# Kernel tuning notes

Hardware: AMD Instinct MI355X
Metric: run time of the kernel (lower is better)

Reference implementation:

```python
import jax, jax.numpy as jnp
import numpy as np
from jax import lax

WIN = 9          # window_size
EPS = 1e-08      # eps


def _box_filter(x):
    """Separable 3D box-mean filter (VALID), equivalent to conv3d with
    ones(WIN,WIN,WIN)/WIN**3. x: (B,1,D',H',W') padded volume."""
    for kshape in ((WIN, 1, 1), (1, WIN, 1), (1, 1, WIN)):
        k = jnp.ones((1, 1) + kshape, x.dtype) / WIN  # (O,I,kd,kh,kw)
        x = lax.conv_general_dilated(
            x, k, window_strides=(1, 1, 1), padding='VALID',
            dimension_numbers=('NCDHW', 'OIDHW', 'NCDHW'))
    return x


def setup_inputs() -> dict:
    key = jax.random.key(0)
    k1, k2 = jax.random.split(key)
    shape = (2, 1, 128, 128, 128)
    fixed = jax.random.uniform(k1, shape, dtype=jnp.float32)
    warped = jax.random.uniform(k2, shape, dtype=jnp.float32)
    return {"fixed": fixed, "warped": warped}


def reference(fixed, warped):
    pad = WIN // 2
    pw = [(0, 0), (0, 0), (pad, pad), (pad, pad), (pad, pad)]
    f = jnp.pad(fixed, pw, mode='reflect')
    w = jnp.pad(warped, pw, mode='reflect')

    mu_f = _box_filter(f)
    mu_w = _box_filter(w)

    sigma_f = jnp.maximum(_box_filter(f * f) - mu_f * mu_f, EPS)
    sigma_w = jnp.maximum(_box_filter(w * w) - mu_w * mu_w, EPS)
    sigma_fw = _box_filter(f * w) - mu_f * mu_w

    denom = jnp.maximum(jnp.sqrt(jnp.maximum(sigma_f * sigma_w, EPS * EPS)), EPS)
    lncc = jnp.clip(sigma_fw / denom, -10.0, 10.0)
    lncc = jnp.nan_to_num(lncc, nan=0.0, posinf=1.0, neginf=-1.0)
    return -jnp.mean(lncc)
```

## Files before the change

### kernel.cpp

```cpp
#include <hip/hip_runtime.h>
#include <math.h>


#define NVOX 4194304
#define SLICE 16384
#define QSCALE (65535.0f / 81.0f)
#define DQ ((float)(81.0 / 65535.0 / 729.0))

__device__ __forceinline__ int refl(int p) {
    return p < 0 ? -p : (p > 127 ? 254 - p : p);
}

__global__ __launch_bounds__(320, 6)
void lncc_wh_kernel(const float* __restrict__ f, const float* __restrict__ w,
                    unsigned short* __restrict__ buf) {
    const int bid   = blockIdx.x;
    const int tile  = bid & 15;
    const int slice = bid >> 4;
    const int th0   = (tile >> 2) << 5;
    const int tw0   = (tile & 3) << 5;
    const int tid   = threadIdx.x;

    __shared__ __align__(16) float tmpT[5][32][44];

    const float* fsl = f + (size_t)slice * SLICE;
    const float* wsl = w + (size_t)slice * SLICE;

    {
        const int i  = tid >> 3;
        const int j0 = (tid & 7) << 2;
        const int row = refl(th0 + i - 4);
        const float* frow = fsl + row * 128;
        const float* wrow = wsl + row * 128;
        const int jb = tw0 + j0 - 4;

        float fv[12], wv[12];
        if (jb >= 0 && jb <= 116) {
            *(float4*)&fv[0] = *(const float4*)&frow[jb];
            *(float4*)&fv[4] = *(const float4*)&frow[jb + 4];
            *(float4*)&fv[8] = *(const float4*)&frow[jb + 8];
            *(float4*)&wv[0] = *(const float4*)&wrow[jb];
            *(float4*)&wv[4] = *(const float4*)&wrow[jb + 4];
            *(float4*)&wv[8] = *(const float4*)&wrow[jb + 8];
        } else {
#pragma unroll
            for (int t = 0; t < 12; ++t) {
                int c = refl(jb + t);
                fv[t] = frow[c];
                wv[t] = wrow[c];
            }
        }

        float sf = 0.f, sw = 0.f, sff = 0.f, sww = 0.f, sfw = 0.f;
#pragma unroll
        for (int t = 0; t < 9; ++t) {
            sf += fv[t]; sw += wv[t];
            sff = fmaf(fv[t], fv[t], sff);
            sww = fmaf(wv[t], wv[t], sww);
            sfw = fmaf(fv[t], wv[t], sfw);
        }
        tmpT[0][j0][i] = sf;  tmpT[1][j0][i] = sw;
        tmpT[2][j0][i] = sff; tmpT[3][j0][i] = sww; tmpT[4][j0][i] = sfw;
#pragma unroll
        for (int k = 1; k < 4; ++k) {
            float fe = fv[k + 8], fx = fv[k - 1];
            float we = wv[k + 8], wx = wv[k - 1];
            sf += fe - fx; sw += we - wx;
            sff = fmaf(fe, fe, sff); sff = fmaf(-fx, fx, sff);
            sww = fmaf(we, we, sww); sww = fmaf(-wx, wx, sww);
            sfw = fmaf(fe, we, sfw); sfw = fmaf(-fx, wx, sfw);
            tmpT[0][j0 + k][i] = sf;  tmpT[1][j0 + k][i] = sw;
            tmpT[2][j0 + k][i] = sff; tmpT[3][j0 + k][i] = sww;
            tmpT[4][j0 + k][i] = sfw;
        }
    }
    __syncthreads();

    if (tid < 256) {
        const int j  = tid & 31;
        const int i0 = (tid >> 5) << 2;
        float acc[5][4];
#pragma unroll
        for (int c = 0; c < 5; ++c) {
            float v[12];
            *(float4*)&v[0] = *(const float4*)&tmpT[c][j][i0];
            *(float4*)&v[4] = *(const float4*)&tmpT[c][j][i0 + 4];
            *(float4*)&v[8] = *(const float4*)&tmpT[c][j][i0 + 8];
            float s = ((v[0] + v[1]) + (v[2] + v[3]))
                    + ((v[4] + v[5]) + (v[6] + v[7])) + v[8];
            acc[c][0] = s;
            s += v[9]  - v[0]; acc[c][1] = s;
            s += v[10] - v[1]; acc[c][2] = s;
            s += v[11] - v[2]; acc[c][3] = s;
        }
        size_t obase = (size_t)slice * SLICE + (size_t)(th0 + i0) * 128 + (tw0 + j);
#pragma unroll
        for (int c = 0; c < 5; ++c)
#pragma unroll
            for (int k = 0; k < 4; ++k)
                buf[(size_t)c * NVOX + obase + (size_t)k * 128] =
                    (unsigned short)fmaf(acc[c][k], QSCALE, 0.5f);
    }
}

__global__ __launch_bounds__(256)
void lncc_d_kernel(const unsigned short* __restrict__ buf,
                   float* __restrict__ partials) {
    const int gtid = blockIdx.x * 256 + threadIdx.x;
    const int wq = gtid & 127;
    const int h  = (gtid >> 7) & 127;
    const int dc = (gtid >> 14) & 15;
    const int b  = gtid >> 18;
    const int d0 = dc << 3;

    float s[5][8];
#pragma unroll
    for (int c = 0; c < 5; ++c) {
        const unsigned short* bc = buf + (size_t)c * NVOX
                                 + (size_t)b * (128 * SLICE)
                                 + (size_t)h * 128 + wq;
        float v[16];
#pragma unroll
        for (int t = 0; t < 16; ++t) {
            int d = refl(d0 - 4 + t);
            v[t] = (float)bc[(size_t)d * SLICE];
        }
        float acc = 0.f;
#pragma unroll
        for (int t = 0; t < 9; ++t) acc += v[t];
        s[c][0] = acc;
#pragma unroll
        for (int j = 1; j < 8; ++j) {
            acc += v[j + 8] - v[j - 1];
            s[c][j] = acc;
        }
    }

    float lsum = 0.f;
#pragma unroll
    for (int j = 0; j < 8; ++j) {
        float mf = s[0][j] * DQ;
        float mw = s[1][j] * DQ;
        float sgf = fmaxf(s[2][j] * DQ - mf * mf, 1e-8f);
        float sgw = fmaxf(s[3][j] * DQ - mw * mw, 1e-8f);
        float sfw = s[4][j] * DQ - mf * mw;
        float denom = fmaxf(sqrtf(fmaxf(sgf * sgw, 1e-16f)), 1e-8f);
        float l = sfw / denom;
        lsum += fminf(fmaxf(l, -10.f), 10.f);
    }

#pragma unroll
    for (int off = 32; off > 0; off >>= 1)
        lsum += __shfl_down(lsum, off, 64);
    __shared__ float red[4];
    int lane = threadIdx.x & 63, wid = threadIdx.x >> 6;
    if (lane == 0) red[wid] = lsum;
    __syncthreads();
    if (threadIdx.x == 0)
        partials[blockIdx.x] = red[0] + red[1] + red[2] + red[3];
}

__global__ __launch_bounds__(256)
void lncc_final_kernel(const float* __restrict__ partials, int n,
                       float* __restrict__ out) {
    __shared__ double rd[256];
    double acc = 0.0;
    for (int i = threadIdx.x; i < n; i += 256) acc += (double)partials[i];
    rd[threadIdx.x] = acc;
    __syncthreads();
    for (int s = 128; s > 0; s >>= 1) {
        if (threadIdx.x < s) rd[threadIdx.x] += rd[threadIdx.x + s];
        __syncthreads();
    }
    if (threadIdx.x == 0) out[0] = (float)(-rd[0] / (double)NVOX);
}

extern "C" void kernel_launch(void* const* d_in, const int* in_sizes, int n_in,
                              void* d_out, int out_size, void* d_ws, size_t ws_size,
                              hipStream_t stream) {
    const float* f = (const float*)d_in[0];
    const float* w = (const float*)d_in[1];
    float* out = (float*)d_out;

    unsigned short* buf = (unsigned short*)d_ws;
    float* partials = (float*)((char*)d_ws + (size_t)5 * NVOX * 2);

    lncc_wh_kernel<<<4096, 320, 0, stream>>>(f, w, buf);
    lncc_d_kernel<<<2048, 256, 0, stream>>>(buf, partials);
    lncc_final_kernel<<<1, 256, 0, stream>>>(partials, 2048, out);
}
```

Before: 47.33 us.

## Process eight depth slices per block with register double-buffered prefetch

```diff
diff --git a/kernel.cpp b/kernel.cpp
--- a/kernel.cpp
+++ b/kernel.cpp
@@ -11,46 +11,36 @@
     return p < 0 ? -p : (p > 127 ? 254 - p : p);
 }
 
-__global__ __launch_bounds__(320, 6)
-void lncc_wh_kernel(const float* __restrict__ f, const float* __restrict__ w,
-                    unsigned short* __restrict__ buf) {
-    const int bid   = blockIdx.x;
-    const int tile  = bid & 15;
-    const int slice = bid >> 4;
-    const int th0   = (tile >> 2) << 5;
-    const int tw0   = (tile & 3) << 5;
-    const int tid   = threadIdx.x;
-
-    __shared__ __align__(16) float tmpT[5][32][44];
-
-    const float* fsl = f + (size_t)slice * SLICE;
-    const float* wsl = w + (size_t)slice * SLICE;
-
+__device__ __forceinline__ void load_slice(const float* __restrict__ fsl,
+                                           const float* __restrict__ wsl,
+                                           int rowoff, int jb,
+                                           float fv[12], float wv[12]) {
+    const float* frow = fsl + rowoff;
+    const float* wrow = wsl + rowoff;
+    if (jb >= 0 && jb <= 116) {
+        *(float4*)&fv[0] = *(const float4*)&frow[jb];
+        *(float4*)&fv[4] = *(const float4*)&frow[jb + 4];
+        *(float4*)&fv[8] = *(const float4*)&frow[jb + 8];
+        *(float4*)&wv[0] = *(const float4*)&wrow[jb];
+        *(float4*)&wv[4] = *(const float4*)&wrow[jb + 4];
+        *(float4*)&wv[8] = *(const float4*)&wrow[jb + 8];
+    } else {
+#pragma unroll
+        for (int t = 0; t < 12; ++t) {
+            int c = refl(jb + t);
+            fv[t] = frow[c];
+            wv[t] = wrow[c];
+        }
+    }
+}
+
+__device__ __forceinline__ void wh_compute_store(
+        const float fv[12], const float wv[12],
+        float (*tmpT)[32][44], int tid, int th0, int tw0, int slice,
+        unsigned short* __restrict__ buf) {
     {
         const int i  = tid >> 3;
         const int j0 = (tid & 7) << 2;
-        const int row = refl(th0 + i - 4);
-        const float* frow = fsl + row * 128;
-        const float* wrow = wsl + row * 128;
-        const int jb = tw0 + j0 - 4;
-
-        float fv[12], wv[12];
-        if (jb >= 0 && jb <= 116) {
-            *(float4*)&fv[0] = *(const float4*)&frow[jb];
-            *(float4*)&fv[4] = *(const float4*)&frow[jb + 4];
-            *(float4*)&fv[8] = *(const float4*)&frow[jb + 8];
-            *(float4*)&wv[0] = *(const float4*)&wrow[jb];
-            *(float4*)&wv[4] = *(const float4*)&wrow[jb + 4];
-            *(float4*)&wv[8] = *(const float4*)&wrow[jb + 8];
-        } else {
-#pragma unroll
-            for (int t = 0; t < 12; ++t) {
-                int c = refl(jb + t);
-                fv[t] = frow[c];
-                wv[t] = wrow[c];
-            }
-        }
-
         float sf = 0.f, sw = 0.f, sff = 0.f, sww = 0.f, sfw = 0.f;
 #pragma unroll
         for (int t = 0; t < 9; ++t) {
@@ -101,6 +91,46 @@
                 buf[(size_t)c * NVOX + obase + (size_t)k * 128] =
                     (unsigned short)fmaf(acc[c][k], QSCALE, 0.5f);
     }
+    __syncthreads();
+}
+
+__global__ __launch_bounds__(320, 2)
+void lncc_wh_kernel(const float* __restrict__ f, const float* __restrict__ w,
+                    unsigned short* __restrict__ buf) {
+    const int bid  = (blockIdx.x & 7) * 64 + (blockIdx.x >> 3);
+    const int tile = bid & 15;
+    const int dg   = (bid >> 4) & 15;
+    const int b    = bid >> 8;
+    const int th0  = (tile >> 2) << 5;
+    const int tw0  = (tile & 3) << 5;
+    const int d0   = dg << 3;
+    const int tid  = threadIdx.x;
+
+    __shared__ __align__(16) float tmpT[5][32][44];
+
+    const int i      = tid >> 3;
+    const int j0     = (tid & 7) << 2;
+    const int rowoff = refl(th0 + i - 4) * 128;
+    const int jb     = tw0 + j0 - 4;
+    (void)i; (void)j0;
+
+    const float* fb = f + (size_t)b * 128 * SLICE;
+    const float* wb = w + (size_t)b * 128 * SLICE;
+
+    float fA[12], wA[12], fB[12], wB[12];
+
+    load_slice(fb + (size_t)d0 * SLICE, wb + (size_t)d0 * SLICE, rowoff, jb, fA, wA);
+#pragma unroll
+    for (int k = 0; k < 8; k += 2) {
+        const int d = d0 + k;
+        load_slice(fb + (size_t)(d + 1) * SLICE, wb + (size_t)(d + 1) * SLICE,
+                   rowoff, jb, fB, wB);
+        wh_compute_store(fA, wA, tmpT, tid, th0, tw0, b * 128 + d, buf);
+        if (k + 2 < 8)
+            load_slice(fb + (size_t)(d + 2) * SLICE, wb + (size_t)(d + 2) * SLICE,
+                       rowoff, jb, fA, wA);
+        wh_compute_store(fB, wB, tmpT, tid, th0, tw0, b * 128 + d + 1, buf);
+    }
 }
 
 __global__ __launch_bounds__(256)
@@ -185,7 +215,7 @@
     unsigned short* buf = (unsigned short*)d_ws;
     float* partials = (float*)((char*)d_ws + (size_t)5 * NVOX * 2);
 
-    lncc_wh_kernel<<<4096, 320, 0, stream>>>(f, w, buf);
+    lncc_wh_kernel<<<512, 320, 0, stream>>>(f, w, buf);
     lncc_d_kernel<<<2048, 256, 0, stream>>>(buf, partials);
     lncc_final_kernel<<<1, 256, 0, stream>>>(partials, 2048, out);
 }
```

New measurement: 56.34 us. 1.19x slower.
